# Performance work log

Measured on AMD Instinct MI355X. Metric: run time of the kernel, lower is better.

Reference implementation:

```python
import jax, jax.numpy as jnp
import numpy as np
import math

B, S, H, D = 8, 2048, 1024, 64  # batch, seq_len, hidden_dim, head_size

def setup_inputs() -> dict:
    key = jax.random.key(0)
    ks = jax.random.split(key, 7)
    lim = 1.0 / math.sqrt(H)  # torch Linear default init bound
    return {
        "x":  jax.random.normal(ks[0], (B, S, H), dtype=jnp.float32),
        "Wq": jax.random.uniform(ks[1], (H, D), jnp.float32, -lim, lim),
        "bq": jax.random.uniform(ks[2], (D,),   jnp.float32, -lim, lim),
        "Wk": jax.random.uniform(ks[3], (H, D), jnp.float32, -lim, lim),
        "bk": jax.random.uniform(ks[4], (D,),   jnp.float32, -lim, lim),
        "Wv": jax.random.uniform(ks[5], (H, D), jnp.float32, -lim, lim),
        "bv": jax.random.uniform(ks[6], (D,),   jnp.float32, -lim, lim),
    }

def reference(x, Wq, bq, Wk, bk, Wv, bv):
    # x: [B, S, H]
    q = x @ Wq + bq          # [B, S, D]
    k = x @ Wk + bk          # [B, S, D]
    v = x @ Wv + bv          # [B, S, D]
    scores = jnp.einsum("bsd,btd->bst", q, k)       # [B, S, S]
    causal = jnp.tril(jnp.ones((S, S), dtype=bool))
    scores = jnp.where(causal, scores, -jnp.inf)
    # NOTE: original module (faithfully) applies softmax FIRST, then divides
    # by sqrt(hidden_dim) -- it does NOT scale logits before softmax.
    weight = jax.nn.softmax(scores, axis=-1) / jnp.sqrt(jnp.float32(x.shape[-1]))
    # dropout p=0.0 -> identity
    return jnp.einsum("bst,btd->bsd", weight, v)     # [B, S, D]
```

## Files before the change

kernel.cpp:

```cpp
#include <hip/hip_runtime.h>


typedef float     f32x4 __attribute__((ext_vector_type(4)));
typedef _Float16  f16x8 __attribute__((ext_vector_type(8)));
typedef _Float16  f16x4 __attribute__((ext_vector_type(4)));

template<bool V> struct BoolT { static constexpr bool value = V; };

__global__ __launch_bounds__(256) void wt_prep(const float* __restrict__ Wq,
                                               const float* __restrict__ Wk,
                                               const float* __restrict__ Wv,
                                               _Float16* __restrict__ WtF) {
  const int w  = blockIdx.x >> 4;
  const int kt = blockIdx.x & 15;
  const float* src = (w == 0) ? Wq : (w == 1 ? Wk : Wv);
  __shared__ _Float16 ls[64][72];
  const int t = threadIdx.x;
  {
    int rr = t >> 4;
    int c4 = (t & 15) * 4;
    #pragma unroll
    for (int ri = 0; ri < 4; ++ri) {
      int k = rr + ri * 16;
      f32x4 f = *(const f32x4*)&src[(size_t)(kt * 64 + k) * 64 + c4];
      #pragma unroll
      for (int j = 0; j < 4; ++j) ls[k][c4 + j] = (_Float16)f[j];
    }
  }
  __syncthreads();
  const int lane = t & 63, l16 = lane & 15, quad = lane >> 4;
  #pragma unroll
  for (int h = 0; h < 2; ++h) {
    int fid     = h * 4 + (t >> 6);
    int kstep_l = fid >> 2;
    int ntl     = fid & 3;
    int nt      = w * 4 + ntl;
    int kstep   = kt * 2 + kstep_l;
    f16x8 o;
    #pragma unroll
    for (int j = 0; j < 8; ++j) o[j] = ls[kstep_l * 32 + quad * 8 + j][ntl * 16 + l16];
    *(f16x8*)&WtF[((size_t)(kstep * 12 + nt) * 64 + lane) * 8] = o;
  }
}

__global__ __launch_bounds__(512, 4) void qkv_gemm(const float* __restrict__ x,
                                                   const _Float16* __restrict__ WtF,
                                                   const float* __restrict__ bq,
                                                   const float* __restrict__ bk,
                                                   const float* __restrict__ bv,
                                                   _Float16* __restrict__ qo,
                                                   _Float16* __restrict__ ko,
                                                   _Float16* __restrict__ vt) {
  __shared__ _Float16 xs[32 * 1024];
  const int tid  = threadIdx.x;
  const int wave = tid >> 6, lane = tid & 63;
  const int l16  = lane & 15, quad = lane >> 4;
  const int mhalf = wave >> 2;
  const int ngrp  = wave & 3;
  const int bid   = blockIdx.x;
  const int m0    = (((bid & 7) << 6) + (bid >> 3)) * 32;

  {
    int row   = tid >> 4;
    int cbase = (tid & 15) * 4;
    const float* xrow = x + (size_t)(m0 + row) * 1024;
    int key = row & 7;
    #pragma unroll
    for (int j = 0; j < 16; ++j) {
      int col = cbase + j * 64;
      f32x4 f = *(const f32x4*)&xrow[col];
      f16x4 hh;
      #pragma unroll
      for (int e = 0; e < 4; ++e) hh[e] = (_Float16)f[e];
      int g   = col >> 3;
      int sub = col & 7;
      *(f16x4*)&xs[(size_t)row * 1024 + (size_t)((g ^ key) << 3) + sub] = hh;
    }
  }
  __syncthreads();

  f32x4 acc0 = (f32x4){0.f,0.f,0.f,0.f};
  f32x4 acc1 = (f32x4){0.f,0.f,0.f,0.f};
  f32x4 acc2 = (f32x4){0.f,0.f,0.f,0.f};

  const int arow = mhalf * 16 + l16;
  const _Float16* abase = xs + (size_t)arow * 1024;
  const int akey = arow & 7;
  const _Float16* wbase = WtF + ((size_t)(ngrp * 3) * 64 + lane) * 8;

  #pragma unroll 4
  for (int kstep = 0; kstep < 32; ++kstep) {
    f16x8 a = *(const f16x8*)(abase + (((kstep * 4 + quad) ^ akey) << 3));
    const _Float16* wk = wbase + (size_t)kstep * (12 * 64 * 8);
    f16x8 b0 = *(const f16x8*)(wk);
    f16x8 b1 = *(const f16x8*)(wk + 512);
    f16x8 b2 = *(const f16x8*)(wk + 1024);
    acc0 = __builtin_amdgcn_mfma_f32_16x16x32_f16(a, b0, acc0, 0, 0, 0);
    acc1 = __builtin_amdgcn_mfma_f32_16x16x32_f16(a, b1, acc1, 0, 0, 0);
    acc2 = __builtin_amdgcn_mfma_f32_16x16x32_f16(a, b2, acc2, 0, 0, 0);
  }

  f32x4 accs[3] = {acc0, acc1, acc2};
  #pragma unroll
  for (int i = 0; i < 3; ++i) {
    int nt  = ngrp * 3 + i;
    int col = nt * 16 + l16;
    float bias = (nt < 4) ? bq[col] : (nt < 8) ? bk[col - 64] : bv[col - 128];
    #pragma unroll
    for (int r = 0; r < 4; ++r) {
      int m = m0 + mhalf * 16 + quad * 4 + r;
      _Float16 hv = (_Float16)(accs[i][r] + bias);
      if (nt < 4)      qo[(size_t)m * 64 + col] = hv;
      else if (nt < 8) ko[(size_t)m * 64 + (col - 64)] = hv;
      else {
        int b = m >> 11, s = m & 2047;
        vt[((size_t)b * 64 + (col - 128)) * 2048 + s] = hv;
      }
    }
  }
}

__global__ __launch_bounds__(256, 3) void attn_part(const _Float16* __restrict__ q,
                                                    const _Float16* __restrict__ k,
                                                    const _Float16* __restrict__ vt,
                                                    float* __restrict__ po,
                                                    float* __restrict__ pml) {
  const int tid  = threadIdx.x;
  const int wave = tid >> 6, lane = tid & 63;
  const int l16  = lane & 15, quad = lane >> 4;
  const int item = blockIdx.x * 4 + wave;

  const int b = item / 1088;
  const int r = item - b * 1088;
  int g = 0;
  {
    int lo = 0, hi = 16;
    while (lo < hi) {
      int mid = (lo + hi + 1) >> 1;
      if (4 * mid * (mid + 1) <= r) lo = mid; else hi = mid - 1;
    }
    g = lo;
  }
  const int rr    = r - 4 * g * (g + 1);
  const int n     = g + 1;
  const int tile  = rr / n;
  const int c     = rr - tile * n;
  const int qt    = 8 * g + tile;
  const int q0    = qt * 16;
  const int kv0   = c * 128;
  const int kvlen = min(128, q0 + 16 - kv0);

  __shared__ _Float16 P[4][16][136];
  __shared__ float    ob[4][16][68];

  const _Float16* qb = q  + (size_t)b * 2048 * 64;
  const _Float16* kb = k  + (size_t)b * 2048 * 64;
  const _Float16* vb = vt + (size_t)b * 64 * 2048;

  f16x8 qf0 = *(const f16x8*)&qb[(q0 + l16) * 64 + quad * 8];
  f16x8 qf1 = *(const f16x8*)&qb[(q0 + l16) * 64 + 32 + quad * 8];

  const float L2E = 1.44269504088896340736f;
  const int qrow  = q0 + l16;

  float m, l;
  f32x4 o[4];

  auto body = [&](auto fullc) {
    constexpr bool FULL = decltype(fullc)::value;

    f16x8 kf[8][2];
    #pragma unroll
    for (int t = 0; t < 8; ++t)
      if (FULL || t * 16 < kvlen) {
        kf[t][0] = *(const f16x8*)&kb[(kv0 + t * 16 + l16) * 64 + quad * 8];
        kf[t][1] = *(const f16x8*)&kb[(kv0 + t * 16 + l16) * 64 + 32 + quad * 8];
      }
    f16x8 vf[4][4];
    #pragma unroll
    for (int ks = 0; ks < 4; ++ks)
      if (FULL || ks * 32 < kvlen) {
        #pragma unroll
        for (int dt = 0; dt < 4; ++dt)
          vf[ks][dt] = *(const f16x8*)&vb[(size_t)(dt * 16 + l16) * 2048 + kv0 + ks * 32 + quad * 8];
      }

    f32x4 sc[8];
    #pragma unroll
    for (int t = 0; t < 8; ++t) {
      const int kvc = kv0 + t * 16;
      f32x4 cc;
      if (FULL || t * 16 < kvlen) {
        cc = (f32x4){0.f, 0.f, 0.f, 0.f};
        cc = __builtin_amdgcn_mfma_f32_16x16x32_f16(kf[t][0], qf0, cc, 0, 0, 0);
        cc = __builtin_amdgcn_mfma_f32_16x16x32_f16(kf[t][1], qf1, cc, 0, 0, 0);
        if (kvc + 15 > q0) {
          #pragma unroll
          for (int rr2 = 0; rr2 < 4; ++rr2)
            if (kvc + quad * 4 + rr2 > qrow) cc[rr2] = -1e30f;
        }
      } else {
        cc = (f32x4){-1e30f, -1e30f, -1e30f, -1e30f};
      }
      sc[t] = cc;
    }

    float mx = -1e30f;
    #pragma unroll
    for (int t = 0; t < 8; ++t)
      mx = fmaxf(mx, fmaxf(fmaxf(sc[t][0], sc[t][1]), fmaxf(sc[t][2], sc[t][3])));
    mx = fmaxf(mx, __shfl_xor(mx, 16, 64));
    mx = fmaxf(mx, __shfl_xor(mx, 32, 64));
    m = mx;

    float s = 0.f;
    #pragma unroll
    for (int t = 0; t < 8; ++t) {
      #pragma unroll
      for (int rr2 = 0; rr2 < 4; ++rr2) sc[t][rr2] = exp2f((sc[t][rr2] - m) * L2E);
      s += (sc[t][0] + sc[t][1]) + (sc[t][2] + sc[t][3]);
    }
    s += __shfl_xor(s, 16, 64);
    s += __shfl_xor(s, 32, 64);
    l = s;

    #pragma unroll
    for (int t = 0; t < 8; ++t) {
      f16x4 ph;
      #pragma unroll
      for (int rr2 = 0; rr2 < 4; ++rr2) ph[rr2] = (_Float16)sc[t][rr2];
      *(f16x4*)&P[wave][l16][t * 16 + quad * 4] = ph;
    }
    asm volatile("s_waitcnt lgkmcnt(0)" ::: "memory");

    #pragma unroll
    for (int i = 0; i < 4; ++i) o[i] = (f32x4){0.f, 0.f, 0.f, 0.f};
    #pragma unroll
    for (int ks = 0; ks < 4; ++ks)
      if (FULL || ks * 32 < kvlen) {
        f16x8 pf = *(const f16x8*)&P[wave][l16][ks * 32 + quad * 8];
        #pragma unroll
        for (int dt = 0; dt < 4; ++dt)
          o[dt] = __builtin_amdgcn_mfma_f32_16x16x32_f16(vf[ks][dt], pf, o[dt], 0, 0, 0);
      }
  };
  if (kvlen == 128) body(BoolT<true>{});
  else              body(BoolT<false>{});

  #pragma unroll
  for (int dt = 0; dt < 4; ++dt)
    *(f32x4*)&ob[wave][l16][dt * 16 + quad * 4] = o[dt];
  if (quad == 0) {
    pml[(size_t)item * 32 + l16]      = m;
    pml[(size_t)item * 32 + 16 + l16] = l;
  }
  asm volatile("s_waitcnt lgkmcnt(0)" ::: "memory");
  {
    const int row = lane >> 2, c4 = (lane & 3) * 16;
    float* dst = po + (size_t)item * 1024 + row * 64 + c4;
    #pragma unroll
    for (int j = 0; j < 4; ++j)
      *(f32x4*)&dst[j * 4] = *(const f32x4*)&ob[wave][row][c4 + j * 4];
  }
}

__global__ __launch_bounds__(256) void attn_merge(const float* __restrict__ po,
                                                  const float* __restrict__ pml,
                                                  float* __restrict__ out) {
  const int blk = blockIdx.x;
  const int b   = blk >> 7, qt = blk & 127;
  const int g   = qt >> 3, n = g + 1;
  const int base = b * 1088 + 4 * g * (g + 1) + (qt & 7) * n;
  const int t   = threadIdx.x;
  const int qr  = t >> 4, d0 = (t & 15) * 4;
  const float L2E = 1.44269504088896340736f;

  const float* mlp = pml + (size_t)base * 32 + qr;
  float M = -1e30f;
  for (int it = 0; it < n; ++it) M = fmaxf(M, mlp[it * 32]);

  float L = 0.f;
  f32x4 acc = (f32x4){0.f, 0.f, 0.f, 0.f};
  for (int it = 0; it < n; ++it) {
    float w = exp2f((mlp[it * 32] - M) * L2E);
    L += w * mlp[it * 32 + 16];
    f32x4 p = *(const f32x4*)&po[((size_t)(base + it) * 16 + qr) * 64 + d0];
    #pragma unroll
    for (int jj = 0; jj < 4; ++jj) acc[jj] += w * p[jj];
  }
  const float inv = 1.0f / (L * 32.0f);
  f32x4 res;
  #pragma unroll
  for (int jj = 0; jj < 4; ++jj) res[jj] = acc[jj] * inv;
  *(f32x4*)&out[((size_t)b * 2048 + qt * 16 + qr) * 64 + d0] = res;
}

extern "C" void kernel_launch(void* const* d_in, const int* in_sizes, int n_in,
                              void* d_out, int out_size, void* d_ws, size_t ws_size,
                              hipStream_t stream) {
  const float* x  = (const float*)d_in[0];
  const float* Wq = (const float*)d_in[1];
  const float* bq = (const float*)d_in[2];
  const float* Wk = (const float*)d_in[3];
  const float* bk = (const float*)d_in[4];
  const float* Wv = (const float*)d_in[5];
  const float* bv = (const float*)d_in[6];
  float* out = (float*)d_out;

  _Float16* WtF = (_Float16*)d_ws;
  _Float16* qo  = WtF + 192 * 1024;
  _Float16* ko  = qo + 16384 * 64;
  _Float16* vt  = ko + 16384 * 64;
  float*    po  = (float*)(vt + 8 * 64 * 2048);
  float*    pml = po + (size_t)8704 * 1024;

  hipLaunchKernelGGL(wt_prep,    dim3(48),   dim3(256), 0, stream, Wq, Wk, Wv, WtF);
  hipLaunchKernelGGL(qkv_gemm,   dim3(512),  dim3(512), 0, stream, x, WtF, bq, bk, bv, qo, ko, vt);
  hipLaunchKernelGGL(attn_part,  dim3(2176), dim3(256), 0, stream, qo, ko, vt, po, pml);
  hipLaunchKernelGGL(attn_merge, dim3(1024), dim3(256), 0, stream, po, pml, out);
}
```

Before: 168.7 us.

## Remap attention work items so each block shares one KV chunk across four query tiles

Changes the block-to-work mapping so the four waves in a block share the same batch and KV chunk and take four consecutive query tiles. This is meant to improve K/V cache reuse across waves. Batch index is interleaved across adjacent blocks, and the merge kernel now computes scattered item indices to match. It also aliases the P and output staging buffers in shared memory to cut LDS use, and raises the occupancy hint from 3 to 5 blocks per CU, which may force register spills.

New measurement: 219.6 us. 1.3x slower.

```diff
diff --git a/kernel.cpp b/kernel.cpp
--- a/kernel.cpp
+++ b/kernel.cpp
@@ -120,7 +120,7 @@
   }
 }
 
-__global__ __launch_bounds__(256, 3) void attn_part(const _Float16* __restrict__ q,
+__global__ __launch_bounds__(256, 5) void attn_part(const _Float16* __restrict__ q,
                                                     const _Float16* __restrict__ k,
                                                     const _Float16* __restrict__ vt,
                                                     float* __restrict__ po,
@@ -128,30 +128,27 @@
   const int tid  = threadIdx.x;
   const int wave = tid >> 6, lane = tid & 63;
   const int l16  = lane & 15, quad = lane >> 4;
-  const int item = blockIdx.x * 4 + wave;
-
-  const int b = item / 1088;
-  const int r = item - b * 1088;
-  int g = 0;
-  {
-    int lo = 0, hi = 16;
-    while (lo < hi) {
-      int mid = (lo + hi + 1) >> 1;
-      if (4 * mid * (mid + 1) <= r) lo = mid; else hi = mid - 1;
-    }
-    g = lo;
-  }
-  const int rr    = r - 4 * g * (g + 1);
-  const int n     = g + 1;
-  const int tile  = rr / n;
-  const int c     = rr - tile * n;
-  const int qt    = 8 * g + tile;
+  const int x    = blockIdx.x;
+  const int b    = x & 7;
+  const int j    = x >> 3;
+
+  int lo = 0, hi = 15;
+  while (lo < hi) {
+    int mid = (lo + hi + 1) >> 1;
+    if (mid * (33 - mid) <= j) lo = mid; else hi = mid - 1;
+  }
+  const int c     = lo;
+  const int u     = j - c * (33 - c);
+  const int rel   = 4 * u + wave;
+  const int qt    = 8 * c + rel;
   const int q0    = qt * 16;
   const int kv0   = c * 128;
-  const int kvlen = min(128, q0 + 16 - kv0);
-
-  __shared__ _Float16 P[4][16][136];
-  __shared__ float    ob[4][16][68];
+  const int kvlen = min(128, 16 * rel + 16);
+  const int item  = (x << 2) | wave;
+
+  __shared__ __align__(16) unsigned char sbuf[4][4352];
+  _Float16 (*P)[136] = (_Float16 (*)[136])&sbuf[wave][0];
+  float    (*ob)[68] = (float    (*)[68])&sbuf[wave][0];
 
   const _Float16* qb = q  + (size_t)b * 2048 * 64;
   const _Float16* kb = k  + (size_t)b * 2048 * 64;
@@ -229,7 +226,7 @@
       f16x4 ph;
       #pragma unroll
       for (int rr2 = 0; rr2 < 4; ++rr2) ph[rr2] = (_Float16)sc[t][rr2];
-      *(f16x4*)&P[wave][l16][t * 16 + quad * 4] = ph;
+      *(f16x4*)&P[l16][t * 16 + quad * 4] = ph;
     }
     asm volatile("s_waitcnt lgkmcnt(0)" ::: "memory");
 
@@ -238,7 +235,7 @@
     #pragma unroll
     for (int ks = 0; ks < 4; ++ks)
       if (FULL || ks * 32 < kvlen) {
-        f16x8 pf = *(const f16x8*)&P[wave][l16][ks * 32 + quad * 8];
+        f16x8 pf = *(const f16x8*)&P[l16][ks * 32 + quad * 8];
         #pragma unroll
         for (int dt = 0; dt < 4; ++dt)
           o[dt] = __builtin_amdgcn_mfma_f32_16x16x32_f16(vf[ks][dt], pf, o[dt], 0, 0, 0);
@@ -249,7 +246,7 @@
 
   #pragma unroll
   for (int dt = 0; dt < 4; ++dt)
-    *(f32x4*)&ob[wave][l16][dt * 16 + quad * 4] = o[dt];
+    *(f32x4*)&ob[l16][dt * 16 + quad * 4] = o[dt];
   if (quad == 0) {
     pml[(size_t)item * 32 + l16]      = m;
     pml[(size_t)item * 32 + 16 + l16] = l;
@@ -259,8 +256,8 @@
     const int row = lane >> 2, c4 = (lane & 3) * 16;
     float* dst = po + (size_t)item * 1024 + row * 64 + c4;
     #pragma unroll
-    for (int j = 0; j < 4; ++j)
-      *(f32x4*)&dst[j * 4] = *(const f32x4*)&ob[wave][row][c4 + j * 4];
+    for (int jj = 0; jj < 4; ++jj)
+      *(f32x4*)&dst[jj * 4] = *(const f32x4*)&ob[row][c4 + jj * 4];
   }
 }
 
@@ -269,22 +266,29 @@
                                                   float* __restrict__ out) {
   const int blk = blockIdx.x;
   const int b   = blk >> 7, qt = blk & 127;
-  const int g   = qt >> 3, n = g + 1;
-  const int base = b * 1088 + 4 * g * (g + 1) + (qt & 7) * n;
+  const int n   = (qt >> 3) + 1;
   const int t   = threadIdx.x;
   const int qr  = t >> 4, d0 = (t & 15) * 4;
   const float L2E = 1.44269504088896340736f;
 
-  const float* mlp = pml + (size_t)base * 32 + qr;
+  int items[16];
+  #pragma unroll 4
+  for (int c = 0; c < n; ++c) {
+    int rel = qt - 8 * c;
+    items[c] = (((c * (33 - c) + (rel >> 2)) * 8 + b) << 2) | (rel & 3);
+  }
+
   float M = -1e30f;
-  for (int it = 0; it < n; ++it) M = fmaxf(M, mlp[it * 32]);
+  for (int it = 0; it < n; ++it)
+    M = fmaxf(M, pml[(size_t)items[it] * 32 + qr]);
 
   float L = 0.f;
   f32x4 acc = (f32x4){0.f, 0.f, 0.f, 0.f};
   for (int it = 0; it < n; ++it) {
-    float w = exp2f((mlp[it * 32] - M) * L2E);
-    L += w * mlp[it * 32 + 16];
-    f32x4 p = *(const f32x4*)&po[((size_t)(base + it) * 16 + qr) * 64 + d0];
+    const float* mlp = pml + (size_t)items[it] * 32;
+    float w = exp2f((mlp[qr] - M) * L2E);
+    L += w * mlp[16 + qr];
+    f32x4 p = *(const f32x4*)&po[((size_t)items[it] * 16 + qr) * 64 + d0];
     #pragma unroll
     for (int jj = 0; jj < 4; ++jj) acc[jj] += w * p[jj];
   }
```
